# Performance work log

Measured on AMD Instinct MI355X. Metric: run time of the kernel, lower is better.

Reference implementation:

```python
import jax, jax.numpy as jnp
import numpy as np

N_FFT = 256
HOP = 64
K = 2       # top-k experts
E = 8       # num experts


def conv1d(x, w, b, stride, pad):
    # x: [B, Cin, L], w: [Cout, Cin, Kw]
    y = jax.lax.conv_general_dilated(x, w, (stride,), [(pad, pad)],
                                     dimension_numbers=('NCH', 'OIH', 'NCH'))
    return y + b[None, :, None]


def stft_mag(x):
    # torch.stft(center=True, pad_mode='reflect', hann window, onesided)
    pad = N_FFT // 2
    xp = jnp.pad(x, ((0, 0), (pad, pad)), mode='reflect')
    n_frames = 1 + (xp.shape[1] - N_FFT) // HOP
    idx = jnp.arange(n_frames)[:, None] * HOP + jnp.arange(N_FFT)[None, :]
    win = 0.5 - 0.5 * jnp.cos(2.0 * jnp.pi * jnp.arange(N_FFT) / N_FFT)  # periodic hann
    frames = xp[:, idx] * win            # [B, F, n_fft]
    return jnp.abs(jnp.fft.rfft(frames, axis=-1))  # [B, F, n_fft//2+1]


def expert_fwd(x, wa3, ba3, wb3, bb3, wa5, ba5, wb5, bb5, wa7, ba7, wb7, bb7):
    # MultiScalePyramidBranch: 3 parallel conv branches (k=3/5/7), 2 conv layers each
    xc = x[:, None, :]  # [B, 1, L]
    outs = []
    for wa, ba, wb, bb in ((wa3, ba3, wb3, bb3), (wa5, ba5, wb5, bb5), (wa7, ba7, wb7, bb7)):
        h = jax.nn.relu(conv1d(xc, wa, ba, 2, wa.shape[-1] // 2))
        h = jax.nn.relu(conv1d(h, wb, bb, 2, 1))
        outs.append(h)
    return jnp.concatenate(outs, axis=1)  # [B, 192, L//4]


def moe_forward(x, Wg1, bg1, Wg2, bg2, Wg3, bg3, ew):
    # gating on frequency domain (stft is computed under no_grad in the original)
    mag = stft_mag(jax.lax.stop_gradient(x))
    pooled = mag.mean(axis=1)                     # adaptive_avg_pool1d(.,1) over frames
    h = jax.nn.relu(pooled @ Wg1 + bg1)
    h = jax.nn.relu(h @ Wg2 + bg2)
    logits = h @ Wg3 + bg3                        # [B, E]
    vals, inds = jax.lax.top_k(logits, K)
    w = jax.nn.softmax(vals, axis=1)              # softmax over the top-k weights
    # vectorized dispatch: run all experts on the whole batch, then gather+combine
    all_out = jax.vmap(expert_fwd, in_axes=(None,) + (0,) * 12)(x, *ew)  # [E, B, C, T]
    B = x.shape[0]
    bidx = jnp.arange(B)
    out = jnp.zeros_like(all_out[0])
    for j in range(K):
        out = out + w[:, j, None, None] * all_out[inds[:, j], bidx]
    return out


def setup_inputs() -> dict:
    key = jax.random.key(0)
    ks = jax.random.split(key, 20)

    def p(k, shape, s=0.02):
        return (s * jax.random.normal(k, shape)).astype(jnp.float32)

    inp = {'x': jax.random.normal(ks[0], (64, 4096), dtype=jnp.float32)}
    inp['Wg1'] = p(ks[1], (129, 256)); inp['bg1'] = jnp.zeros((256,), jnp.float32)
    inp['Wg2'] = p(ks[2], (256, 128)); inp['bg2'] = jnp.zeros((128,), jnp.float32)
    inp['Wg3'] = p(ks[3], (128, E));   inp['bg3'] = jnp.zeros((E,), jnp.float32)
    i = 4
    for ksz in (3, 5, 7):
        inp['wa%d' % ksz] = p(ks[i], (E, 64, 1, ksz)); i += 1
        inp['ba%d' % ksz] = jnp.zeros((E, 64), jnp.float32)
        inp['wb%d' % ksz] = p(ks[i], (E, 64, 64, 3)); i += 1
        inp['bb%d' % ksz] = jnp.zeros((E, 64), jnp.float32)
    return inp


def reference(x, Wg1, bg1, Wg2, bg2, Wg3, bg3,
              wa3, ba3, wb3, bb3, wa5, ba5, wb5, bb5, wa7, ba7, wb7, bb7):
    ew = (wa3, ba3, wb3, bb3, wa5, ba5, wb5, bb5, wa7, ba7, wb7, bb7)
    return moe_forward(x, Wg1, bg1, Wg2, bg2, Wg3, bg3, ew)
```

## Files before the change

### kernel.cpp

```cpp
#include <hip/hip_runtime.h>
#include <math.h>

#define NFFT 256
#define NBINS 129
#define HOP 64
#define NFRAMES 65
#define NB 64
#define LX 4096
#define LH 2048
#define LY 1024
#define NCH 64
#define NBR 3
#define NE 8

#define NFG 13
#define PART_STRIDE 132
#define WTF_OFF 440320
#define WTF_PER 98304
#define IW_OFF 1031168

typedef __attribute__((ext_vector_type(8))) short short8;
typedef __attribute__((ext_vector_type(4))) float floatx4;

__device__ __forceinline__ unsigned short bf16r(float f) {
    unsigned u = __builtin_bit_cast(unsigned, f);
    u += 0x7FFFu + ((u >> 16) & 1u);
    return (unsigned short)(u >> 16);
}

__global__ __launch_bounds__(128) void stft_kernel(
    const float* __restrict__ x,
    const float* __restrict__ wb3, const float* __restrict__ wb5,
    const float* __restrict__ wb7, unsigned short* __restrict__ wTf,
    float* __restrict__ part) {
    __shared__ float xw[NFFT];
    const int g = blockIdx.x, b = blockIdx.y;
    const int tid = threadIdx.x;

    {
        int bid = b * NFG + g;
        for (int fi = bid * 128 + tid; fi < 3 * WTF_PER; fi += NB * NFG * 128) {
            int br = fi / WTF_PER, r = fi % WTF_PER;
            int e = r / 12288;
            int r2 = r % 12288;
            int mw = r2 / 3072;
            int r3 = r2 % 3072;
            int i = r3 / 1024;
            int r4 = r3 % 1024;
            int kb = r4 / 512;
            int r5 = r4 % 512;
            int lane = r5 / 8, j = r5 % 8;
            int c2 = mw * 16 + (lane & 15);
            int cl = kb * 32 + (lane >> 4) * 8 + j;
            const float* src = (br == 0) ? wb3 : (br == 1) ? wb5 : wb7;
            wTf[fi] = bf16r(src[((e * 64 + c2) * 64 + cl) * 3 + i]);
        }
    }

    const int k = tid;
    float ang = (float)(2.0 * 3.14159265358979323846 / 256.0) * (float)k;
    float s1, c1;
    sincosf(ang, &s1, &c1);

    float acck = 0.f, accN = 0.f;
    for (int f0 = 0; f0 < 5; ++f0) {
        int f = g * 5 + f0;
        __syncthreads();
        for (int n = tid; n < NFFT; n += 128) {
            float a2 = (float)(2.0 * 3.14159265358979323846 / 256.0) * (float)n;
            float sn, cn;
            sincosf(a2, &sn, &cn);
            float win = 0.5f - 0.5f * cn;
            int q = f * HOP + n - 128;
            int xi = q < 0 ? -q : (q >= LX ? (2 * LX - 2 - q) : q);
            xw[n] = x[b * LX + xi] * win;
        }
        __syncthreads();
        float c = 1.f, s = 0.f;
        float re = 0.f, im = 0.f;
        float reN = 0.f, sgn = 1.f;
        for (int n = 0; n < NFFT; ++n) {
            float v = xw[n];
            re += v * c;
            im += v * s;
            reN += v * sgn;
            sgn = -sgn;
            float t = c * c1 - s * s1;
            s = c * s1 + s * c1;
            c = t;
        }
        acck += sqrtf(re * re + im * im);
        accN += fabsf(reN);
    }
    float* prow = part + (b * NFG + g) * PART_STRIDE;
    prow[k] = acck;
    if (tid == 0) prow[128] = accN;
}

__global__ __launch_bounds__(256) void gating_kernel(
    const float* __restrict__ part,
    const float* __restrict__ Wg1, const float* __restrict__ bg1,
    const float* __restrict__ Wg2, const float* __restrict__ bg2,
    const float* __restrict__ Wg3, const float* __restrict__ bg3,
    int* __restrict__ inds, float* __restrict__ wts) {
    __shared__ float pl[NBINS];
    __shared__ float h1[256];
    __shared__ float h2[128];
    __shared__ float lg[NE];
    const int b = blockIdx.x, tid = threadIdx.x;

    if (tid < NBINS) {
        float s = 0.f;
        for (int g = 0; g < NFG; ++g)
            s += part[(b * NFG + g) * PART_STRIDE + tid];
        pl[tid] = s * (1.0f / (float)NFRAMES);
    }
    __syncthreads();
    {
        float s = bg1[tid];
        for (int k = 0; k < NBINS; ++k) s += pl[k] * Wg1[k * 256 + tid];
        h1[tid] = fmaxf(s, 0.f);
    }
    __syncthreads();
    if (tid < 128) {
        float s = bg2[tid];
        for (int k = 0; k < 256; ++k) s += h1[k] * Wg2[k * 128 + tid];
        h2[tid] = fmaxf(s, 0.f);
    }
    __syncthreads();
    if (tid < NE) {
        float s = bg3[tid];
        for (int k = 0; k < 128; ++k) s += h2[k] * Wg3[k * NE + tid];
        lg[tid] = s;
    }
    __syncthreads();
    if (tid == 0) {
        int i0 = 0;
        float v0 = lg[0];
        for (int i = 1; i < NE; ++i)
            if (lg[i] > v0) { v0 = lg[i]; i0 = i; }
        int i1 = -1;
        float v1 = -3.0e38f;
        for (int i = 0; i < NE; ++i) {
            if (i == i0) continue;
            if (lg[i] > v1) { v1 = lg[i]; i1 = i; }
        }
        float e1 = expf(v1 - v0);
        float w0 = 1.f / (1.f + e1);
        inds[b * 2 + 0] = i0;
        inds[b * 2 + 1] = i1;
        wts[b * 2 + 0] = w0;
        wts[b * 2 + 1] = e1 * w0;
    }
}

#define UT 128
#define HPR 68
#define HROWS 258

template <int KSZ>
__device__ __attribute__((always_inline)) void expert_body(
    const float* __restrict__ x,
    const float* __restrict__ wa, const float* __restrict__ ba,
    const float* __restrict__ bb, const unsigned short* __restrict__ wTfbr,
    const int* __restrict__ inds, const float* __restrict__ wts,
    float* __restrict__ out, int br, short* hp) {
    const int u0 = blockIdx.x * UT;
    const int b = blockIdx.z;
    const int tid = threadIdx.x;
    const int lane = tid & 63;
    const int quad = lane >> 4;
    const int l15 = lane & 15;
    const int wv = __builtin_amdgcn_readfirstlane(tid >> 6);
    const int mw = wv & 3;
    const int nh = wv >> 2;
    const int pad = KSZ >> 1;
    const int t0 = 2 * u0 - 1;
    const int x0 = 2 * t0 - pad;

    const float* xp = x + b * LX;

    float fin[4][4];
#pragma unroll
    for (int q = 0; q < 4; ++q)
#pragma unroll
        for (int r = 0; r < 4; ++r) fin[q][r] = 0.f;

#pragma unroll 1
    for (int slot = 0; slot < 2; ++slot) {
        const int e = __builtin_amdgcn_readfirstlane(inds[b * 2 + slot]);
        const float wj = wts[b * 2 + slot];

        float wr[KSZ];
#pragma unroll
        for (int i = 0; i < KSZ; ++i) wr[i] = wa[(e * NCH + lane) * KSZ + i];
        const float bv = ba[e * NCH + lane];

        __syncthreads();

#pragma unroll 1
        for (int it = 0; it < 9; ++it) {
            int tb = wv + 8 * it;
            if (tb > 64) break;
            int base = x0 + 8 * tb;
            float xr[16];
            if (base >= 0 && base + 15 < LX) {
#pragma unroll
                for (int ii = 0; ii < 16; ++ii) xr[ii] = xp[base + ii];
            } else {
#pragma unroll
                for (int ii = 0; ii < 16; ++ii) {
                    int xi = base + ii;
                    xr[ii] = (xi >= 0 && xi < LX) ? xp[xi] : 0.f;
                }
            }
#pragma unroll
            for (int m = 0; m < 4; ++m) {
                int tl = 4 * tb + m;
                if (tl > 257) continue;
                int t = t0 + tl;
                float s = bv;
#pragma unroll
                for (int i = 0; i < KSZ; ++i) s += wr[i] * xr[2 * m + i];
                float h = (t >= 0 && t < LH) ? fmaxf(s, 0.f) : 0.f;
                hp[tl * HPR + lane] = (short)bf16r(h);
            }
        }
        __syncthreads();

        float br4[4];
#pragma unroll
        for (int r = 0; r < 4; ++r)
            br4[r] = bb[e * NCH + mw * 16 + quad * 4 + r];

        short8 af[3][2];
        {
            const unsigned short* wbase =
                wTfbr + e * 12288 + mw * 3072 + lane * 8;
#pragma unroll
            for (int i = 0; i < 3; ++i)
#pragma unroll
                for (int kb = 0; kb < 2; ++kb)
                    af[i][kb] = *(const short8*)&wbase[i * 1024 + kb * 512];
        }

#pragma unroll 1
        for (int q = 0; q < 4; ++q) {
            int nt = nh * 4 + q;
            int nb = nt * 16 + l15;
            floatx4 acc = {br4[0], br4[1], br4[2], br4[3]};
#pragma unroll
            for (int i = 0; i < 3; ++i) {
                int tl = 2 * nb + i;
#pragma unroll
                for (int kb = 0; kb < 2; ++kb) {
                    int sb = tl * HPR + kb * 32 + quad * 8;
                    union { short8 v; unsigned long long q2[2]; } B;
                    B.q2[0] = *(const unsigned long long*)&hp[sb];
                    B.q2[1] = *(const unsigned long long*)&hp[sb + 4];
                    acc = __builtin_amdgcn_mfma_f32_16x16x32_bf16(
                        af[i][kb], B.v, acc, 0, 0, 0);
                }
            }
#pragma unroll
            for (int r = 0; r < 4; ++r)
                fin[q][r] += wj * fmaxf(acc[r], 0.f);
        }
    }

#pragma unroll
    for (int q = 0; q < 4; ++q) {
        int u = u0 + (nh * 4 + q) * 16 + l15;
#pragma unroll
        for (int r = 0; r < 4; ++r) {
            int c2 = mw * 16 + quad * 4 + r;
            out[(long)(b * 192 + br * 64 + c2) * LY + u] = fin[q][r];
        }
    }
}

__global__ __launch_bounds__(512, 2) void expert_kernel(
    const float* __restrict__ x,
    const float* __restrict__ wa3, const float* __restrict__ ba3,
    const float* __restrict__ bb3,
    const float* __restrict__ wa5, const float* __restrict__ ba5,
    const float* __restrict__ bb5,
    const float* __restrict__ wa7, const float* __restrict__ ba7,
    const float* __restrict__ bb7,
    const unsigned short* __restrict__ wTf,
    const int* __restrict__ inds, const float* __restrict__ wts,
    float* __restrict__ out) {
    __shared__ short hp[HROWS * HPR];

    const int br = blockIdx.y;
    if (br == 0)
        expert_body<3>(x, wa3, ba3, bb3, wTf, inds, wts, out, 0, hp);
    else if (br == 1)
        expert_body<5>(x, wa5, ba5, bb5, wTf + WTF_PER, inds, wts, out, 1, hp);
    else
        expert_body<7>(x, wa7, ba7, bb7, wTf + 2 * WTF_PER, inds, wts, out, 2, hp);
}

extern "C" void kernel_launch(void* const* d_in, const int* in_sizes, int n_in,
                              void* d_out, int out_size, void* d_ws, size_t ws_size,
                              hipStream_t stream) {
    const float* x   = (const float*)d_in[0];
    const float* Wg1 = (const float*)d_in[1];
    const float* bg1 = (const float*)d_in[2];
    const float* Wg2 = (const float*)d_in[3];
    const float* bg2 = (const float*)d_in[4];
    const float* Wg3 = (const float*)d_in[5];
    const float* bg3 = (const float*)d_in[6];
    const float* wa3 = (const float*)d_in[7];
    const float* ba3 = (const float*)d_in[8];
    const float* wb3 = (const float*)d_in[9];
    const float* bb3 = (const float*)d_in[10];
    const float* wa5 = (const float*)d_in[11];
    const float* ba5 = (const float*)d_in[12];
    const float* wb5 = (const float*)d_in[13];
    const float* bb5 = (const float*)d_in[14];
    const float* wa7 = (const float*)d_in[15];
    const float* ba7 = (const float*)d_in[16];
    const float* wb7 = (const float*)d_in[17];
    const float* bb7 = (const float*)d_in[18];

    float* part = (float*)d_ws;
    unsigned short* wTf = (unsigned short*)((char*)d_ws + WTF_OFF);
    int* inds = (int*)((char*)d_ws + IW_OFF);
    float* wts = (float*)((char*)d_ws + IW_OFF + 512);

    stft_kernel<<<dim3(NFG, NB), 128, 0, stream>>>(x, wb3, wb5, wb7, wTf, part);
    gating_kernel<<<NB, 256, 0, stream>>>(part, Wg1, bg1, Wg2, bg2, Wg3, bg3,
                                          inds, wts);
    expert_kernel<<<dim3(LY / UT, NBR, NB), 512, 0, stream>>>(
        x, wa3, ba3, bb3, wa5, ba5, bb5, wa7, ba7, bb7, wTf,
        inds, wts, (float*)d_out);
}
```

Before: 200.5 us.

## Fuse STFT and gating MLP via atomic pooling and last-block election

Merges the STFT and gating kernels into one launch. Each block now handles a single frame, giving 65x64 blocks instead of 13x64, and atomically adds its magnitudes into a pooled buffer. The last block per batch row, found through an atomic counter, runs the gating MLP and top-k. This drops one kernel launch and the partial-sum pass and adds parallelism, at the cost of a memset launch, atomics, and float-summation order that is no longer deterministic.

Measured after the change: 250.3 us. 1.25x slower.

```diff
diff --git a/kernel.cpp b/kernel.cpp
--- a/kernel.cpp
+++ b/kernel.cpp
@@ -13,11 +13,12 @@
 #define NBR 3
 #define NE 8
 
-#define NFG 13
-#define PART_STRIDE 132
-#define WTF_OFF 440320
+#define POOLED_BYTES 33024
+#define CNT_OFF 33024
+#define ZERO_BYTES 33280
+#define WTF_OFF 33792
 #define WTF_PER 98304
-#define IW_OFF 1031168
+#define IW_OFF 623616
 
 typedef __attribute__((ext_vector_type(8))) short short8;
 typedef __attribute__((ext_vector_type(4))) float floatx4;
@@ -28,18 +29,24 @@
     return (unsigned short)(u >> 16);
 }
 
-__global__ __launch_bounds__(128) void stft_kernel(
+__global__ __launch_bounds__(128) void stft_gating_kernel(
     const float* __restrict__ x,
     const float* __restrict__ wb3, const float* __restrict__ wb5,
     const float* __restrict__ wb7, unsigned short* __restrict__ wTf,
-    float* __restrict__ part) {
+    float* __restrict__ pooled, unsigned int* __restrict__ cnt,
+    const float* __restrict__ Wg1, const float* __restrict__ bg1,
+    const float* __restrict__ Wg2, const float* __restrict__ bg2,
+    const float* __restrict__ Wg3, const float* __restrict__ bg3,
+    int* __restrict__ inds, float* __restrict__ wts) {
     __shared__ float xw[NFFT];
-    const int g = blockIdx.x, b = blockIdx.y;
+    __shared__ int islast;
+    const int f = blockIdx.x, b = blockIdx.y;
     const int tid = threadIdx.x;
 
     {
-        int bid = b * NFG + g;
-        for (int fi = bid * 128 + tid; fi < 3 * WTF_PER; fi += NB * NFG * 128) {
+        int bid = b * NFRAMES + f;
+        for (int fi = bid * 128 + tid; fi < 3 * WTF_PER;
+             fi += NB * NFRAMES * 128) {
             int br = fi / WTF_PER, r = fi % WTF_PER;
             int e = r / 12288;
             int r2 = r % 12288;
@@ -57,81 +64,79 @@
         }
     }
 
+    for (int n = tid; n < NFFT; n += 128) {
+        float a2 = (float)(2.0 * 3.14159265358979323846 / 256.0) * (float)n;
+        float sn, cn;
+        sincosf(a2, &sn, &cn);
+        float win = 0.5f - 0.5f * cn;
+        int q = f * HOP + n - 128;
+        int xi = q < 0 ? -q : (q >= LX ? (2 * LX - 2 - q) : q);
+        xw[n] = x[b * LX + xi] * win;
+    }
+    __syncthreads();
+
     const int k = tid;
     float ang = (float)(2.0 * 3.14159265358979323846 / 256.0) * (float)k;
     float s1, c1;
     sincosf(ang, &s1, &c1);
-
-    float acck = 0.f, accN = 0.f;
-    for (int f0 = 0; f0 < 5; ++f0) {
-        int f = g * 5 + f0;
-        __syncthreads();
-        for (int n = tid; n < NFFT; n += 128) {
-            float a2 = (float)(2.0 * 3.14159265358979323846 / 256.0) * (float)n;
-            float sn, cn;
-            sincosf(a2, &sn, &cn);
-            float win = 0.5f - 0.5f * cn;
-            int q = f * HOP + n - 128;
-            int xi = q < 0 ? -q : (q >= LX ? (2 * LX - 2 - q) : q);
-            xw[n] = x[b * LX + xi] * win;
-        }
-        __syncthreads();
-        float c = 1.f, s = 0.f;
-        float re = 0.f, im = 0.f;
-        float reN = 0.f, sgn = 1.f;
-        for (int n = 0; n < NFFT; ++n) {
-            float v = xw[n];
-            re += v * c;
-            im += v * s;
-            reN += v * sgn;
-            sgn = -sgn;
-            float t = c * c1 - s * s1;
-            s = c * s1 + s * c1;
-            c = t;
-        }
-        acck += sqrtf(re * re + im * im);
-        accN += fabsf(reN);
-    }
-    float* prow = part + (b * NFG + g) * PART_STRIDE;
-    prow[k] = acck;
-    if (tid == 0) prow[128] = accN;
-}
-
-__global__ __launch_bounds__(256) void gating_kernel(
-    const float* __restrict__ part,
-    const float* __restrict__ Wg1, const float* __restrict__ bg1,
-    const float* __restrict__ Wg2, const float* __restrict__ bg2,
-    const float* __restrict__ Wg3, const float* __restrict__ bg3,
-    int* __restrict__ inds, float* __restrict__ wts) {
+    float c = 1.f, s = 0.f;
+    float re = 0.f, im = 0.f, rN = 0.f;
+    for (int n = 0; n < NFFT; n += 2) {
+        float v0 = xw[n], v1 = xw[n + 1];
+        re = fmaf(v0, c, re);
+        im = fmaf(v0, s, im);
+        rN += v0;
+        float t = c * c1 - s * s1;
+        s = c * s1 + s * c1;
+        c = t;
+        re = fmaf(v1, c, re);
+        im = fmaf(v1, s, im);
+        rN -= v1;
+        t = c * c1 - s * s1;
+        s = c * s1 + s * c1;
+        c = t;
+    }
+    atomicAdd(&pooled[b * NBINS + k], sqrtf(re * re + im * im));
+    if (tid == 0) atomicAdd(&pooled[b * NBINS + 128], fabsf(rN));
+
+    if (tid == 0) {
+        __threadfence();
+        unsigned old = atomicAdd(&cnt[b], 1u);
+        islast = (old == NFRAMES - 1) ? 1 : 0;
+    }
+    __syncthreads();
+    if (!islast) return;
+    __threadfence();
+
     __shared__ float pl[NBINS];
     __shared__ float h1[256];
     __shared__ float h2[128];
     __shared__ float lg[NE];
-    const int b = blockIdx.x, tid = threadIdx.x;
-
-    if (tid < NBINS) {
-        float s = 0.f;
-        for (int g = 0; g < NFG; ++g)
-            s += part[(b * NFG + g) * PART_STRIDE + tid];
-        pl[tid] = s * (1.0f / (float)NFRAMES);
+
+    pl[tid] = __hip_atomic_load(&pooled[b * NBINS + tid], __ATOMIC_RELAXED,
+                                __HIP_MEMORY_SCOPE_AGENT) *
+              (1.0f / (float)NFRAMES);
+    if (tid == 0)
+        pl[128] = __hip_atomic_load(&pooled[b * NBINS + 128], __ATOMIC_RELAXED,
+                                    __HIP_MEMORY_SCOPE_AGENT) *
+                  (1.0f / (float)NFRAMES);
+    __syncthreads();
+    for (int o = tid; o < 256; o += 128) {
+        float v = bg1[o];
+        for (int kk = 0; kk < NBINS; ++kk) v += pl[kk] * Wg1[kk * 256 + o];
+        h1[o] = fmaxf(v, 0.f);
     }
     __syncthreads();
     {
-        float s = bg1[tid];
-        for (int k = 0; k < NBINS; ++k) s += pl[k] * Wg1[k * 256 + tid];
-        h1[tid] = fmaxf(s, 0.f);
-    }
-    __syncthreads();
-    if (tid < 128) {
-        float s = bg2[tid];
-        for (int k = 0; k < 256; ++k) s += h1[k] * Wg2[k * 128 + tid];
-        h2[tid] = fmaxf(s, 0.f);
+        float v = bg2[tid];
+        for (int kk = 0; kk < 256; ++kk) v += h1[kk] * Wg2[kk * 128 + tid];
+        h2[tid] = fmaxf(v, 0.f);
     }
     __syncthreads();
     if (tid < NE) {
-        float s = bg3[tid];
-        for (int k = 0; k < 128; ++k) s += h2[k] * Wg3[k * NE + tid];
-        lg[tid] = s;
+        float v = bg3[tid];
+        for (int kk = 0; kk < 128; ++kk) v += h2[kk] * Wg3[kk * NE + tid];
+        lg[tid] = v;
     }
     __syncthreads();
     if (tid == 0) {
@@ -324,14 +329,16 @@
     const float* wb7 = (const float*)d_in[17];
     const float* bb7 = (const float*)d_in[18];
 
-    float* part = (float*)d_ws;
+    float* pooled = (float*)d_ws;
+    unsigned int* cnt = (unsigned int*)((char*)d_ws + CNT_OFF);
     unsigned short* wTf = (unsigned short*)((char*)d_ws + WTF_OFF);
     int* inds = (int*)((char*)d_ws + IW_OFF);
     float* wts = (float*)((char*)d_ws + IW_OFF + 512);
 
-    stft_kernel<<<dim3(NFG, NB), 128, 0, stream>>>(x, wb3, wb5, wb7, wTf, part);
-    gating_kernel<<<NB, 256, 0, stream>>>(part, Wg1, bg1, Wg2, bg2, Wg3, bg3,
-                                          inds, wts);
+    hipMemsetAsync(d_ws, 0, ZERO_BYTES, stream);
+    stft_gating_kernel<<<dim3(NFRAMES, NB), 128, 0, stream>>>(
+        x, wb3, wb5, wb7, wTf, pooled, cnt,
+        Wg1, bg1, Wg2, bg2, Wg3, bg3, inds, wts);
     expert_kernel<<<dim3(LY / UT, NBR, NB), 512, 0, stream>>>(
         x, wa3, ba3, bb3, wa5, ba5, bb5, wa7, ba7, bb7, wTf,
         inds, wts, (float*)d_out);
```

## Split STFT into one block per frame with radix-4 decomposed DFT and atomics

Applied to the files above, without the earlier changes.

The STFT kernel now launches one block per frame (65 per batch row) instead of 13 blocks that each looped over 5 frames. This raises parallelism, and the per-frame partial magnitudes are accumulated into the existing partial rows with atomicAdd after a memset clears that buffer. Each thread's 256-point DFT is split into four interleaved 64-sample quarter sums with independent twiddle recurrences, recombined through k-dependent quarter-turn phase factors. This gives more independent FMA chains and vectorised shared-memory reads. The cost is an extra memset launch, atomic contention on the partial buffer, and floating-point summation order that changes between runs.

Measured after the change: 179.8 us. 1.11x faster.

```diff
diff --git a/kernel.cpp b/kernel.cpp
--- a/kernel.cpp
+++ b/kernel.cpp
@@ -15,6 +15,7 @@
 
 #define NFG 13
 #define PART_STRIDE 132
+#define PART_ZERO 440320
 #define WTF_OFF 440320
 #define WTF_PER 98304
 #define IW_OFF 1031168
@@ -34,12 +35,13 @@
     const float* __restrict__ wb7, unsigned short* __restrict__ wTf,
     float* __restrict__ part) {
     __shared__ float xw[NFFT];
-    const int g = blockIdx.x, b = blockIdx.y;
+    const int f = blockIdx.x, b = blockIdx.y;
     const int tid = threadIdx.x;
 
     {
-        int bid = b * NFG + g;
-        for (int fi = bid * 128 + tid; fi < 3 * WTF_PER; fi += NB * NFG * 128) {
+        int bid = b * NFRAMES + f;
+        for (int fi = bid * 128 + tid; fi < 3 * WTF_PER;
+             fi += NB * NFRAMES * 128) {
             int br = fi / WTF_PER, r = fi % WTF_PER;
             int e = r / 12288;
             int r2 = r % 12288;
@@ -57,44 +59,69 @@
         }
     }
 
+    for (int n = tid; n < NFFT; n += 128) {
+        float a2 = (float)(2.0 * 3.14159265358979323846 / 256.0) * (float)n;
+        float sn, cn;
+        sincosf(a2, &sn, &cn);
+        float win = 0.5f - 0.5f * cn;
+        int q = f * HOP + n - 128;
+        int xi = q < 0 ? -q : (q >= LX ? (2 * LX - 2 - q) : q);
+        xw[n] = x[b * LX + xi] * win;
+    }
+    __syncthreads();
+
     const int k = tid;
     float ang = (float)(2.0 * 3.14159265358979323846 / 256.0) * (float)k;
     float s1, c1;
     sincosf(ang, &s1, &c1);
 
-    float acck = 0.f, accN = 0.f;
-    for (int f0 = 0; f0 < 5; ++f0) {
-        int f = g * 5 + f0;
-        __syncthreads();
-        for (int n = tid; n < NFFT; n += 128) {
-            float a2 = (float)(2.0 * 3.14159265358979323846 / 256.0) * (float)n;
-            float sn, cn;
-            sincosf(a2, &sn, &cn);
-            float win = 0.5f - 0.5f * cn;
-            int q = f * HOP + n - 128;
-            int xi = q < 0 ? -q : (q >= LX ? (2 * LX - 2 - q) : q);
-            xw[n] = x[b * LX + xi] * win;
-        }
-        __syncthreads();
-        float c = 1.f, s = 0.f;
-        float re = 0.f, im = 0.f;
-        float reN = 0.f, sgn = 1.f;
-        for (int n = 0; n < NFFT; ++n) {
-            float v = xw[n];
-            re += v * c;
-            im += v * s;
-            reN += v * sgn;
-            sgn = -sgn;
-            float t = c * c1 - s * s1;
-            s = c * s1 + s * c1;
-            c = t;
-        }
-        acck += sqrtf(re * re + im * im);
-        accN += fabsf(reN);
-    }
-    float* prow = part + (b * NFG + g) * PART_STRIDE;
-    prow[k] = acck;
-    if (tid == 0) prow[128] = accN;
+    float A0 = 0.f, B0 = 0.f, A1 = 0.f, B1 = 0.f;
+    float A2 = 0.f, B2 = 0.f, A3 = 0.f, B3 = 0.f;
+    float c0 = 1.f, s0 = 0.f, cc1 = 1.f, ss1 = 0.f;
+    float cc2 = 1.f, ss2 = 0.f, cc3 = 1.f, ss3 = 0.f;
+    float rNe = 0.f, rNo = 0.f;
+
+#pragma unroll 4
+    for (int mq = 0; mq < 16; ++mq) {
+        float4 v0 = *(const float4*)&xw[4 * mq];
+        float4 v1 = *(const float4*)&xw[64 + 4 * mq];
+        float4 v2 = *(const float4*)&xw[128 + 4 * mq];
+        float4 v3 = *(const float4*)&xw[192 + 4 * mq];
+        float e0[4] = {v0.x, v0.y, v0.z, v0.w};
+        float e1[4] = {v1.x, v1.y, v1.z, v1.w};
+        float e2[4] = {v2.x, v2.y, v2.z, v2.w};
+        float e3[4] = {v3.x, v3.y, v3.z, v3.w};
+#pragma unroll
+        for (int mm = 0; mm < 4; ++mm) {
+            float t;
+            A0 = fmaf(e0[mm], c0, A0);  B0 = fmaf(e0[mm], s0, B0);
+            A1 = fmaf(e1[mm], cc1, A1); B1 = fmaf(e1[mm], ss1, B1);
+            A2 = fmaf(e2[mm], cc2, A2); B2 = fmaf(e2[mm], ss2, B2);
+            A3 = fmaf(e3[mm], cc3, A3); B3 = fmaf(e3[mm], ss3, B3);
+            if ((mm & 1) == 0) rNe += e0[mm] + e1[mm] + e2[mm] + e3[mm];
+            else               rNo += e0[mm] + e1[mm] + e2[mm] + e3[mm];
+            t = c0 * c1 - s0 * s1;   s0 = fmaf(c0, s1, s0 * c1);   c0 = t;
+            t = cc1 * c1 - ss1 * s1; ss1 = fmaf(cc1, s1, ss1 * c1); cc1 = t;
+            t = cc2 * c1 - ss2 * s1; ss2 = fmaf(cc2, s1, ss2 * c1); cc2 = t;
+            t = cc3 * c1 - ss3 * s1; ss3 = fmaf(cc3, s1, ss3 * c1); cc3 = t;
+        }
+    }
+
+    float re = A0, im = B0;
+    float Aj[3] = {A1, A2, A3};
+    float Bj[3] = {B1, B2, B3};
+#pragma unroll
+    for (int j = 1; j < 4; ++j) {
+        int ph = (j * k) & 3;
+        float cf = (ph == 0) ? 1.f : (ph == 2) ? -1.f : 0.f;
+        float sf = (ph == 1) ? 1.f : (ph == 3) ? -1.f : 0.f;
+        re += cf * Aj[j - 1] - sf * Bj[j - 1];
+        im += sf * Aj[j - 1] + cf * Bj[j - 1];
+    }
+
+    float* prow = part + (b * NFG + f / 5) * PART_STRIDE;
+    atomicAdd(&prow[k], sqrtf(re * re + im * im));
+    if (tid == 0) atomicAdd(&prow[128], fabsf(rNe - rNo));
 }
 
 __global__ __launch_bounds__(256) void gating_kernel(
@@ -118,19 +145,19 @@
     __syncthreads();
     {
         float s = bg1[tid];
-        for (int k = 0; k < NBINS; ++k) s += pl[k] * Wg1[k * 256 + tid];
+        for (int kk = 0; kk < NBINS; ++kk) s += pl[kk] * Wg1[kk * 256 + tid];
         h1[tid] = fmaxf(s, 0.f);
     }
     __syncthreads();
     if (tid < 128) {
         float s = bg2[tid];
-        for (int k = 0; k < 256; ++k) s += h1[k] * Wg2[k * 128 + tid];
+        for (int kk = 0; kk < 256; ++kk) s += h1[kk] * Wg2[kk * 128 + tid];
         h2[tid] = fmaxf(s, 0.f);
     }
     __syncthreads();
     if (tid < NE) {
         float s = bg3[tid];
-        for (int k = 0; k < 128; ++k) s += h2[k] * Wg3[k * NE + tid];
+        for (int kk = 0; kk < 128; ++kk) s += h2[kk] * Wg3[kk * NE + tid];
         lg[tid] = s;
     }
     __syncthreads();
@@ -329,7 +356,9 @@
     int* inds = (int*)((char*)d_ws + IW_OFF);
     float* wts = (float*)((char*)d_ws + IW_OFF + 512);
 
-    stft_kernel<<<dim3(NFG, NB), 128, 0, stream>>>(x, wb3, wb5, wb7, wTf, part);
+    hipMemsetAsync(d_ws, 0, PART_ZERO, stream);
+    stft_kernel<<<dim3(NFRAMES, NB), 128, 0, stream>>>(x, wb3, wb5, wb7, wTf,
+                                                       part);
     gating_kernel<<<NB, 256, 0, stream>>>(part, Wg1, bg1, Wg2, bg2, Wg3, bg3,
                                           inds, wts);
     expert_kernel<<<dim3(LY / UT, NBR, NB), 512, 0, stream>>>(
```
